# Optimization experiments

Hardware: AMD Instinct MI355X
Metric: run time of the kernel (lower is better)

## Reference

```python
import jax, jax.numpy as jnp
import numpy as np

B, T, C = 2, 4096, 768
H = 12
D = C // H  # head_size = 64


def setup_inputs() -> dict:
    key = jax.random.key(0)
    k1, k2, k3 = jax.random.split(key, 3)
    x = jax.random.normal(k1, (B, T, C), dtype=jnp.float32)
    w_attn = jax.random.normal(k2, (C, 3 * C), dtype=jnp.float32) * (C ** -0.5)
    b_attn = jnp.zeros((3 * C,), dtype=jnp.float32)
    w_proj = jax.random.normal(k3, (C, C), dtype=jnp.float32) * (C ** -0.5)
    b_proj = jnp.zeros((C,), dtype=jnp.float32)
    return {"x": x, "w_attn": w_attn, "b_attn": b_attn, "w_proj": w_proj, "b_proj": b_proj}


def reference(x, w_attn, b_attn, w_proj, b_proj):
    Bx, Tx, Cx = x.shape
    # fused QKV projection
    qkv = x @ w_attn + b_attn  # (B, T, 3C)
    q, k, v = jnp.split(qkv, 3, axis=2)
    # (B, H, T, D)
    q = q.reshape(Bx, Tx, H, D).transpose(0, 2, 1, 3)
    k = k.reshape(Bx, Tx, H, D).transpose(0, 2, 1, 3)
    v = v.reshape(Bx, Tx, H, D).transpose(0, 2, 1, 3)
    scale = 1.0 / jnp.sqrt(jnp.asarray(D, dtype=x.dtype))
    scores = jnp.einsum('bhqd,bhkd->bhqk', q, k) * scale  # (B, H, T, T)
    causal = jnp.tril(jnp.ones((Tx, Tx), dtype=bool))
    scores = jnp.where(causal, scores, jnp.asarray(-jnp.inf, dtype=scores.dtype))
    attn = jax.nn.softmax(scores, axis=-1)
    y = jnp.einsum('bhqk,bhkd->bhqd', attn, v)  # (B, H, T, D)
    y = y.transpose(0, 2, 1, 3).reshape(Bx, Tx, Cx)
    return y @ w_proj + b_proj
```

## Files before the change

kernel.cpp:

```cpp
#include <hip/hip_runtime.h>
#include <stdint.h>

#define B_   2
#define T_   4096
#define C_   768
#define H_   12
#define D_   64
#define BH_  24
#define M_   8192
#define K_   768
#define N1_  2304

#define NEG_BIG (-1.0e30f)
#define QSCALE 0.18033688011112042f

typedef short bf16x8 __attribute__((ext_vector_type(8)));
typedef float f32x4  __attribute__((ext_vector_type(4)));
typedef float f32x16 __attribute__((ext_vector_type(16)));
typedef uint32_t u32x4 __attribute__((ext_vector_type(4)));
typedef int i32x2 __attribute__((ext_vector_type(2)));

typedef const __attribute__((address_space(1))) void* as1cv;
typedef __attribute__((address_space(3))) void*       as3v;

__device__ __forceinline__ void gload_lds16(const void* g, void* l) {
  __builtin_amdgcn_global_load_lds((as1cv)g, (as3v)l, 16, 0, 0);
}

__device__ __forceinline__ unsigned short f2bf(float f) {
  uint32_t x = __builtin_bit_cast(uint32_t, f);
  uint32_t r = (x + 0x7fffu + ((x >> 16) & 1u)) >> 16;
  return (unsigned short)r;
}

__device__ __forceinline__ unsigned short f2bf_hu(float f) {
  return (unsigned short)((__builtin_bit_cast(uint32_t, f) + 0x8000u) >> 16);
}

#if __has_builtin(__builtin_amdgcn_perm)
__device__ __forceinline__ uint32_t pack_hu(float lo, float hi) {
  uint32_t a = __builtin_bit_cast(uint32_t, lo) + 0x8000u;
  uint32_t b = __builtin_bit_cast(uint32_t, hi) + 0x8000u;
  return __builtin_amdgcn_perm(b, a, 0x07060302u);
}
#else
__device__ __forceinline__ uint32_t pack_hu(float lo, float hi) {
  uint32_t a = __builtin_bit_cast(uint32_t, lo) + 0x8000u;
  uint32_t b = __builtin_bit_cast(uint32_t, hi) + 0x8000u;
  return (b & 0xFFFF0000u) | (a >> 16);
}
#endif

#if __has_builtin(__builtin_amdgcn_permlane32_swap)
#define HAVE_PLSWAP 1
#else
#define HAVE_PLSWAP 0
#endif

#if __has_builtin(__builtin_amdgcn_exp2f)
__device__ __forceinline__ float fast_exp2(float x) { return __builtin_amdgcn_exp2f(x); }
#else
__device__ __forceinline__ float fast_exp2(float x) { return __expf(x * 0.69314718056f); }
#endif

__global__ void cast_kernel(const float* __restrict__ in, unsigned short* __restrict__ out, int n4) {
  int idx = blockIdx.x * blockDim.x + threadIdx.x;
  int stride = gridDim.x * blockDim.x;
  for (int i = idx; i < n4; i += stride) {
    float4 v = reinterpret_cast<const float4*>(in)[i];
    ushort4 o;
    o.x = f2bf(v.x); o.y = f2bf(v.y); o.z = f2bf(v.z); o.w = f2bf(v.w);
    reinterpret_cast<ushort4*>(out)[i] = o;
  }
}

__global__ void transpose_cast(const float* __restrict__ in, unsigned short* __restrict__ out,
                               int K, int N) {
  __shared__ float tile[32][33];
  const int tx = threadIdx.x, ty = threadIdx.y;
  const int n = blockIdx.x * 32 + tx;
  #pragma unroll
  for (int r = 0; r < 4; ++r) {
    int k = blockIdx.y * 32 + ty + r * 8;
    tile[ty + r * 8][tx] = in[(size_t)k * N + n];
  }
  __syncthreads();
  const int k = blockIdx.y * 32 + tx;
  #pragma unroll
  for (int r = 0; r < 4; ++r) {
    int nn = blockIdx.x * 32 + ty + r * 8;
    out[(size_t)nn * K + k] = f2bf(tile[tx][ty + r * 8]);
  }
}

template <int MODE>
__global__ __launch_bounds__(256) void gemm_kernel(
    const unsigned short* __restrict__ A, const unsigned short* __restrict__ BT,
    const float* __restrict__ bias,
    unsigned short* __restrict__ o0, unsigned short* __restrict__ o1,
    unsigned short* __restrict__ o2, float* __restrict__ fo) {
  __shared__ __align__(16) unsigned short Al[128 * 32];
  __shared__ __align__(16) unsigned short Bl[128 * 32];
  const int tid = threadIdx.x;
  const int w = tid >> 6, lane = tid & 63;
  const int g = lane >> 4, c16 = lane & 15;
  const int wr = w >> 1, wc = w & 1;
  const int m0 = blockIdx.x * 128, n0 = blockIdx.y * 128;

  f32x4 acc[4][4] = {};

  for (int k0 = 0; k0 < K_; k0 += 32) {
    __syncthreads();
    #pragma unroll
    for (int q = 0; q < 2; ++q) {
      const int ch = (w * 2 + q) * 64 + lane;
      const int row = ch >> 2, kb = ch & 3;
      gload_lds16(A  + (size_t)(m0 + row) * K_ + k0 + kb * 8, &Al[(w * 2 + q) * 512]);
      gload_lds16(BT + (size_t)(n0 + row) * K_ + k0 + kb * 8, &Bl[(w * 2 + q) * 512]);
    }
    __syncthreads();
    bf16x8 af[4], bfr[4];
    #pragma unroll
    for (int i = 0; i < 4; ++i) {
      af[i]  = *reinterpret_cast<const bf16x8*>(&Al[(wr * 64 + i * 16 + c16) * 32 + g * 8]);
      bfr[i] = *reinterpret_cast<const bf16x8*>(&Bl[(wc * 64 + i * 16 + c16) * 32 + g * 8]);
    }
    #pragma unroll
    for (int i = 0; i < 4; ++i)
      #pragma unroll
      for (int j = 0; j < 4; ++j)
        acc[i][j] = __builtin_amdgcn_mfma_f32_16x16x32_bf16(af[i], bfr[j], acc[i][j], 0, 0, 0);
  }

  const int which = (MODE == 0) ? (n0 / 768) : 0;
  #pragma unroll
  for (int i = 0; i < 4; ++i) {
    const int mbase = m0 + wr * 64 + i * 16 + g * 4;
    #pragma unroll
    for (int j2 = 0; j2 < 4; ++j2) {
      const int n = n0 + wc * 64 + j2 * 16 + c16;
      const float bv = bias[n];
      #pragma unroll
      for (int j = 0; j < 4; ++j) {
        float v = acc[i][j2][j] + bv;
        const int mm = mbase + j;
        if constexpr (MODE == 0) {
          const int cc = n - which * 768;
          const int hh = cc >> 6, dd = cc & 63;
          const int bb = mm >> 12, tt = mm & 4095;
          const size_t bh = (size_t)bb * H_ + hh;
          const size_t hb = bh * T_ * D_;
          if (which == 0) {
            o0[hb + (size_t)tt * D_ + dd] = f2bf_hu(v * QSCALE);
          } else if (which == 1) {
            const int addr = ((tt >> 5) * 4 + (dd >> 4)) * 512 +
                             ((tt & 31) + ((dd >> 3) & 1) * 32) * 8 + (dd & 7);
            o1[hb + addr] = f2bf_hu(v);
          } else {
            const int addr = (tt >> 6) * 4096 + (dd >> 5) * 2048 +
                             ((tt >> 4) & 3) * 512 +
                             ((dd & 31) + ((tt >> 3) & 1) * 32) * 8 + (tt & 7);
            o2[hb + addr] = f2bf_hu(v);
          }
        } else {
          fo[(size_t)mm * 768 + n] = v;
        }
      }
    }
  }
}

__global__ __launch_bounds__(256, 2) void attn_kernel(
    const unsigned short* __restrict__ Qb, const unsigned short* __restrict__ Kb,
    const unsigned short* __restrict__ Vt, unsigned short* __restrict__ Yb) {
  __shared__ float Ml[3][64];
  __shared__ float Ll[3][64];
  __shared__ __align__(16) float Yl[3][32][64];

  const int tidx = threadIdx.x;
  const int wv = tidx >> 6;
  const int lane = tidx & 63;
  const int q31 = lane & 31, hi = lane >> 5;
  const int bid = blockIdx.x;
  const int bh = bid % BH_;
  const int strip = (T_ / 32 - 1) - bid / BH_;
  const int q0 = strip * 32;
  const int qg = q0 + q31;

  const int bb = bh / H_, hh = bh % H_;
  const size_t hoff = (size_t)bh * T_ * D_;
  const unsigned short* Qh = Qb + hoff;
  const unsigned short* Kh = Kb + hoff + lane * 8;
  const unsigned short* Vh = Vt + hoff + lane * 8;

  bf16x8 qf[4];
  #pragma unroll
  for (int s = 0; s < 4; ++s)
    qf[s] = *reinterpret_cast<const bf16x8*>(&Qh[(size_t)qg * D_ + s * 16 + hi * 8]);

  float mrun = NEG_BIG, lrun = 0.f;
  f32x16 y0 = {}, y1 = {};

  const int nt = ((q0 + 31) >> 6) + 1;

  bf16x8 kfA[8], kfB[8];

  auto tile_step = [&](bf16x8 (&kfc)[8], bf16x8 (&kfn)[8], int it) {
    const int kv0 = it << 6;

    const unsigned short* vB = Vh + it * 4096;
    bf16x8 vfA[4], vfB[4];
    #pragma unroll
    for (int ks = 0; ks < 4; ++ks) {
      vfA[ks] = *reinterpret_cast<const bf16x8*>(vB + ks * 512);
      vfB[ks] = *reinterpret_cast<const bf16x8*>(vB + 2048 + ks * 512);
    }

    const unsigned short* kN = Kh + it * 4096 + 16384;
    #pragma unroll
    for (int s = 0; s < 8; ++s)
      kfn[s] = *reinterpret_cast<const bf16x8*>(kN + (s >> 2) * 2048 + (s & 3) * 512);

    f32x16 s0 = {}, s1 = {};
    #pragma unroll
    for (int s = 0; s < 4; ++s)
      s0 = __builtin_amdgcn_mfma_f32_32x32x16_bf16(kfc[s], qf[s], s0, 0, 0, 0);
    #pragma unroll
    for (int s = 0; s < 4; ++s)
      s1 = __builtin_amdgcn_mfma_f32_32x32x16_bf16(kfc[4 + s], qf[s], s1, 0, 0, 0);

    if (kv0 + 63 > q0) {
      #pragma unroll
      for (int r = 0; r < 16; ++r) {
        const int kvl = (r & 3) + 8 * (r >> 2) + 4 * hi;
        s0[r] = (kv0 + kvl > qg)      ? NEG_BIG : s0[r];
        s1[r] = (kv0 + 32 + kvl > qg) ? NEG_BIG : s1[r];
      }
    }

    float a[16];
    #pragma unroll
    for (int r = 0; r < 8; ++r) a[r] = fmaxf(s0[2 * r], s0[2 * r + 1]);
    #pragma unroll
    for (int r = 0; r < 8; ++r) a[8 + r] = fmaxf(s1[2 * r], s1[2 * r + 1]);
    #pragma unroll
    for (int st = 8; st > 0; st >>= 1)
      #pragma unroll
      for (int r = 0; r < 16; ++r) if (r < st) a[r] = fmaxf(a[r], a[r + st]);
    float tmax = a[0];
    tmax = fmaxf(tmax, __shfl_xor(tmax, 32));

    if (__any(tmax > mrun + 11.5f)) {
      const float mnew = fmaxf(mrun, tmax);
      const float alpha = fast_exp2(mrun - mnew);
      mrun = mnew;
      lrun *= alpha;
      #pragma unroll
      for (int r = 0; r < 16; ++r) { y0[r] *= alpha; y1[r] *= alpha; }
    }

    #pragma unroll
    for (int r = 0; r < 16; ++r) {
      s0[r] = fast_exp2(s0[r] - mrun);
      s1[r] = fast_exp2(s1[r] - mrun);
    }

    #pragma unroll
    for (int r = 0; r < 8; ++r) a[r] = s0[2 * r] + s0[2 * r + 1];
    #pragma unroll
    for (int r = 0; r < 8; ++r) a[8 + r] = s1[2 * r] + s1[2 * r + 1];
    #pragma unroll
    for (int st = 8; st > 0; st >>= 1)
      #pragma unroll
      for (int r = 0; r < 16; ++r) if (r < st) a[r] = a[r] + a[r + st];
    float rsum = a[0];
    rsum += __shfl_xor(rsum, 32);
    lrun += rsum;

    bf16x8 pf[4];
#if HAVE_PLSWAP
#define MK_PF(KS, SH, GA, HA)                                                 \
    {                                                                         \
      uint32_t g0 = pack_hu(SH[(GA)*4 + 0], SH[(GA)*4 + 1]);                  \
      uint32_t g1 = pack_hu(SH[(GA)*4 + 2], SH[(GA)*4 + 3]);                  \
      uint32_t h0 = pack_hu(SH[(HA)*4 + 0], SH[(HA)*4 + 1]);                  \
      uint32_t h1 = pack_hu(SH[(HA)*4 + 2], SH[(HA)*4 + 3]);                  \
      i32x2 r0 = __builtin_amdgcn_permlane32_swap((int)g0, (int)h0, false, false); \
      i32x2 r1 = __builtin_amdgcn_permlane32_swap((int)g1, (int)h1, false, false); \
      u32x4 t;                                                                \
      t[0] = (uint32_t)r0[0];                                                 \
      t[1] = (uint32_t)r1[0];                                                 \
      t[2] = (uint32_t)r0[1];                                                 \
      t[3] = (uint32_t)r1[1];                                                 \
      pf[KS] = __builtin_bit_cast(bf16x8, t);                                 \
    }
#else
#define MK_PF(KS, SH, GA, HA)                                                 \
    {                                                                         \
      uint32_t g0 = pack_hu(SH[(GA)*4 + 0], SH[(GA)*4 + 1]);                  \
      uint32_t g1 = pack_hu(SH[(GA)*4 + 2], SH[(GA)*4 + 3]);                  \
      uint32_t h0 = pack_hu(SH[(HA)*4 + 0], SH[(HA)*4 + 1]);                  \
      uint32_t h1 = pack_hu(SH[(HA)*4 + 2], SH[(HA)*4 + 3]);                  \
      uint32_t sg0 = (uint32_t)__shfl_xor((int)g0, 32);                       \
      uint32_t sg1 = (uint32_t)__shfl_xor((int)g1, 32);                       \
      uint32_t sh0 = (uint32_t)__shfl_xor((int)h0, 32);                       \
      uint32_t sh1 = (uint32_t)__shfl_xor((int)h1, 32);                       \
      u32x4 t;                                                                \
      t[0] = hi ? sh0 : g0;                                                   \
      t[1] = hi ? sh1 : g1;                                                   \
      t[2] = hi ? h0 : sg0;                                                   \
      t[3] = hi ? h1 : sg1;                                                   \
      pf[KS] = __builtin_bit_cast(bf16x8, t);                                 \
    }
#endif
    MK_PF(0, s0, 0, 1)
    MK_PF(1, s0, 2, 3)
    MK_PF(2, s1, 0, 1)
    MK_PF(3, s1, 2, 3)
#undef MK_PF

    #pragma unroll
    for (int ks = 0; ks < 4; ++ks)
      y0 = __builtin_amdgcn_mfma_f32_32x32x16_bf16(vfA[ks], pf[ks], y0, 0, 0, 0);
    #pragma unroll
    for (int ks = 0; ks < 4; ++ks)
      y1 = __builtin_amdgcn_mfma_f32_32x32x16_bf16(vfB[ks], pf[ks], y1, 0, 0, 0);
  };

  int it = wv;
  if (it < nt) {
    #pragma unroll
    for (int s = 0; s < 8; ++s)
      kfA[s] = *reinterpret_cast<const bf16x8*>(
          Kh + (wv << 12) + (s >> 2) * 2048 + (s & 3) * 512);
    for (;;) {
      tile_step(kfA, kfB, it);
      it += 4; if (it >= nt) break;
      tile_step(kfB, kfA, it);
      it += 4; if (it >= nt) break;
    }
  }

  if (wv > 0) {
    Ml[wv - 1][lane] = mrun;
    Ll[wv - 1][lane] = lrun;
    #pragma unroll
    for (int r = 0; r < 16; ++r) {
      Yl[wv - 1][r][lane] = y0[r];
      Yl[wv - 1][16 + r][lane] = y1[r];
    }
  }
  __syncthreads();
  if (wv == 0) {
    float mp[3];
    float mm = mrun;
    #pragma unroll
    for (int p = 0; p < 3; ++p) { mp[p] = Ml[p][lane]; mm = fmaxf(mm, mp[p]); }
    const float aw = fast_exp2(mrun - mm);
    float ap[3];
    float ll = lrun * aw;
    #pragma unroll
    for (int p = 0; p < 3; ++p) {
      ap[p] = fast_exp2(mp[p] - mm);
      ll += Ll[p][lane] * ap[p];
    }
    const float inv = 1.f / ll;

    const size_t ro = ((size_t)bb * T_ + qg) * C_ + hh * D_;
    #pragma unroll
    for (int q2 = 0; q2 < 4; ++q2) {
      float v[8];
      #pragma unroll
      for (int e = 0; e < 4; ++e) {
        float t0 = y0[q2 * 4 + e] * aw;
        float t1 = y1[q2 * 4 + e] * aw;
        #pragma unroll
        for (int p = 0; p < 3; ++p) {
          t0 += Yl[p][q2 * 4 + e][lane] * ap[p];
          t1 += Yl[p][16 + q2 * 4 + e][lane] * ap[p];
        }
        v[e] = t0 * inv;
        v[4 + e] = t1 * inv;
      }
      uint2 pr0 = {pack_hu(v[0], v[1]), pack_hu(v[2], v[3])};
      *reinterpret_cast<uint2*>(&Yb[ro + q2 * 8 + hi * 4]) = pr0;
      uint2 pr1 = {pack_hu(v[4], v[5]), pack_hu(v[6], v[7])};
      *reinterpret_cast<uint2*>(&Yb[ro + 32 + q2 * 8 + hi * 4]) = pr1;
    }
  }
}

extern "C" void kernel_launch(void* const* d_in, const int* in_sizes, int n_in,
                              void* d_out, int out_size, void* d_ws, size_t ws_size,
                              hipStream_t stream) {
  const float* x      = (const float*)d_in[0];
  const float* w_attn = (const float*)d_in[1];
  const float* b_attn = (const float*)d_in[2];
  const float* w_proj = (const float*)d_in[3];
  const float* b_proj = (const float*)d_in[4];
  float* out = (float*)d_out;

  char* ws = (char*)d_ws;
  size_t off = 0;
  auto alloc = [&](size_t bytes) -> void* {
    void* p = ws + off;
    off += (bytes + 255) & ~(size_t)255;
    return p;
  };
  unsigned short* xb  = (unsigned short*)alloc((size_t)M_ * K_ * 2);
  unsigned short* waT = (unsigned short*)alloc((size_t)N1_ * K_ * 2);
  unsigned short* wpT = (unsigned short*)alloc((size_t)C_ * K_ * 2);
  unsigned short* Qb  = (unsigned short*)alloc((size_t)BH_ * T_ * D_ * 2);
  unsigned short* Kb  = (unsigned short*)alloc((size_t)BH_ * T_ * D_ * 2);
  unsigned short* Vt  = (unsigned short*)alloc((size_t)BH_ * D_ * T_ * 2);
  unsigned short* Yb  = (unsigned short*)alloc((size_t)M_ * C_ * 2);

  cast_kernel<<<1024, 256, 0, stream>>>(x, xb, M_ * K_ / 4);
  transpose_cast<<<dim3(N1_ / 32, K_ / 32), dim3(32, 8), 0, stream>>>(w_attn, waT, K_, N1_);
  transpose_cast<<<dim3(C_ / 32, K_ / 32), dim3(32, 8), 0, stream>>>(w_proj, wpT, K_, C_);

  gemm_kernel<0><<<dim3(M_ / 128, N1_ / 128), 256, 0, stream>>>(
      xb, waT, b_attn, Qb, Kb, Vt, nullptr);

  attn_kernel<<<(T_ / 32) * BH_, 256, 0, stream>>>(Qb, Kb, Vt, Yb);

  gemm_kernel<1><<<dim3(M_ / 128, C_ / 128), 256, 0, stream>>>(
      Yb, wpT, b_proj, nullptr, nullptr, nullptr, out);
}
```

Before: 186.0 us.

## Process 64 queries per attention block to reuse K/V tiles across two query groups

Each attention block now handles two 32-row query groups (64 queries) per wave, sharing every loaded K and V tile between them, and the grid is halved. This halves global K/V traffic per query and gives more MFMA work per load. It also drops the software prefetch of the next K tile, which may expose load latency, and the extra accumulators raise register pressure under the 2-blocks-per-CU launch bound. The diagonal-tile masking is specialised for the 64-row strip.

Measured after the change: 174.8 us. 1.06x faster.

```diff
diff --git a/kernel.cpp b/kernel.cpp
--- a/kernel.cpp
+++ b/kernel.cpp
@@ -173,9 +173,9 @@
 __global__ __launch_bounds__(256, 2) void attn_kernel(
     const unsigned short* __restrict__ Qb, const unsigned short* __restrict__ Kb,
     const unsigned short* __restrict__ Vt, unsigned short* __restrict__ Yb) {
-  __shared__ float Ml[3][64];
-  __shared__ float Ll[3][64];
-  __shared__ __align__(16) float Yl[3][32][64];
+  __shared__ float Ml[3][2][64];
+  __shared__ float Ll[3][2][64];
+  __shared__ __align__(16) float Yl[3][64][64];
 
   const int tidx = threadIdx.x;
   const int wv = tidx >> 6;
@@ -183,9 +183,10 @@
   const int q31 = lane & 31, hi = lane >> 5;
   const int bid = blockIdx.x;
   const int bh = bid % BH_;
-  const int strip = (T_ / 32 - 1) - bid / BH_;
-  const int q0 = strip * 32;
-  const int qg = q0 + q31;
+  const int strip = (T_ / 64 - 1) - bid / BH_;
+  const int q0 = strip * 64;
+  const int qgA = q0 + q31;
+  const int qgB = q0 + 32 + q31;
 
   const int bb = bh / H_, hh = bh % H_;
   const size_t hoff = (size_t)bh * T_ * D_;
@@ -193,199 +194,280 @@
   const unsigned short* Kh = Kb + hoff + lane * 8;
   const unsigned short* Vh = Vt + hoff + lane * 8;
 
-  bf16x8 qf[4];
+  bf16x8 qfA[4], qfB[4];
   #pragma unroll
-  for (int s = 0; s < 4; ++s)
-    qf[s] = *reinterpret_cast<const bf16x8*>(&Qh[(size_t)qg * D_ + s * 16 + hi * 8]);
-
-  float mrun = NEG_BIG, lrun = 0.f;
-  f32x16 y0 = {}, y1 = {};
-
-  const int nt = ((q0 + 31) >> 6) + 1;
-
-  bf16x8 kfA[8], kfB[8];
-
-  auto tile_step = [&](bf16x8 (&kfc)[8], bf16x8 (&kfn)[8], int it) {
+  for (int s = 0; s < 4; ++s) {
+    qfA[s] = *reinterpret_cast<const bf16x8*>(&Qh[(size_t)qgA * D_ + s * 16 + hi * 8]);
+    qfB[s] = *reinterpret_cast<const bf16x8*>(&Qh[(size_t)qgB * D_ + s * 16 + hi * 8]);
+  }
+
+  float mA = NEG_BIG, lA = 0.f, mB = NEG_BIG, lB = 0.f;
+  f32x16 yA0 = {}, yA1 = {}, yB0 = {}, yB1 = {};
+
+  const int nt = strip + 1;
+
+  for (int it = wv; it < nt; it += 4) {
     const int kv0 = it << 6;
 
-    const unsigned short* vB = Vh + it * 4096;
-    bf16x8 vfA[4], vfB[4];
+    const unsigned short* kT = Kh + it * 4096;
+    bf16x8 kf[8];
+    #pragma unroll
+    for (int s = 0; s < 8; ++s)
+      kf[s] = *reinterpret_cast<const bf16x8*>(kT + (s >> 2) * 2048 + (s & 3) * 512);
+
+    const unsigned short* vT = Vh + it * 4096;
+    bf16x8 vlo[4], vhi[4];
     #pragma unroll
     for (int ks = 0; ks < 4; ++ks) {
-      vfA[ks] = *reinterpret_cast<const bf16x8*>(vB + ks * 512);
-      vfB[ks] = *reinterpret_cast<const bf16x8*>(vB + 2048 + ks * 512);
-    }
-
-    const unsigned short* kN = Kh + it * 4096 + 16384;
-    #pragma unroll
-    for (int s = 0; s < 8; ++s)
-      kfn[s] = *reinterpret_cast<const bf16x8*>(kN + (s >> 2) * 2048 + (s & 3) * 512);
-
-    f32x16 s0 = {}, s1 = {};
-    #pragma unroll
-    for (int s = 0; s < 4; ++s)
-      s0 = __builtin_amdgcn_mfma_f32_32x32x16_bf16(kfc[s], qf[s], s0, 0, 0, 0);
-    #pragma unroll
-    for (int s = 0; s < 4; ++s)
-      s1 = __builtin_amdgcn_mfma_f32_32x32x16_bf16(kfc[4 + s], qf[s], s1, 0, 0, 0);
-
-    if (kv0 + 63 > q0) {
+      vlo[ks] = *reinterpret_cast<const bf16x8*>(vT + ks * 512);
+      vhi[ks] = *reinterpret_cast<const bf16x8*>(vT + 2048 + ks * 512);
+    }
+
+    f32x16 sA0 = {}, sA1 = {}, sB0 = {}, sB1 = {};
+    #pragma unroll
+    for (int s = 0; s < 4; ++s) {
+      sA0 = __builtin_amdgcn_mfma_f32_32x32x16_bf16(kf[s], qfA[s], sA0, 0, 0, 0);
+      sB0 = __builtin_amdgcn_mfma_f32_32x32x16_bf16(kf[s], qfB[s], sB0, 0, 0, 0);
+    }
+    #pragma unroll
+    for (int s = 0; s < 4; ++s) {
+      sA1 = __builtin_amdgcn_mfma_f32_32x32x16_bf16(kf[4 + s], qfA[s], sA1, 0, 0, 0);
+      sB1 = __builtin_amdgcn_mfma_f32_32x32x16_bf16(kf[4 + s], qfB[s], sB1, 0, 0, 0);
+    }
+
+    if (it == strip) {
       #pragma unroll
       for (int r = 0; r < 16; ++r) {
         const int kvl = (r & 3) + 8 * (r >> 2) + 4 * hi;
-        s0[r] = (kv0 + kvl > qg)      ? NEG_BIG : s0[r];
-        s1[r] = (kv0 + 32 + kvl > qg) ? NEG_BIG : s1[r];
-      }
-    }
-
-    float a[16];
-    #pragma unroll
-    for (int r = 0; r < 8; ++r) a[r] = fmaxf(s0[2 * r], s0[2 * r + 1]);
-    #pragma unroll
-    for (int r = 0; r < 8; ++r) a[8 + r] = fmaxf(s1[2 * r], s1[2 * r + 1]);
-    #pragma unroll
-    for (int st = 8; st > 0; st >>= 1)
-      #pragma unroll
-      for (int r = 0; r < 16; ++r) if (r < st) a[r] = fmaxf(a[r], a[r + st]);
-    float tmax = a[0];
-    tmax = fmaxf(tmax, __shfl_xor(tmax, 32));
-
-    if (__any(tmax > mrun + 11.5f)) {
-      const float mnew = fmaxf(mrun, tmax);
-      const float alpha = fast_exp2(mrun - mnew);
-      mrun = mnew;
-      lrun *= alpha;
-      #pragma unroll
-      for (int r = 0; r < 16; ++r) { y0[r] *= alpha; y1[r] *= alpha; }
-    }
-
-    #pragma unroll
-    for (int r = 0; r < 16; ++r) {
-      s0[r] = fast_exp2(s0[r] - mrun);
-      s1[r] = fast_exp2(s1[r] - mrun);
-    }
-
-    #pragma unroll
-    for (int r = 0; r < 8; ++r) a[r] = s0[2 * r] + s0[2 * r + 1];
-    #pragma unroll
-    for (int r = 0; r < 8; ++r) a[8 + r] = s1[2 * r] + s1[2 * r + 1];
-    #pragma unroll
-    for (int st = 8; st > 0; st >>= 1)
-      #pragma unroll
-      for (int r = 0; r < 16; ++r) if (r < st) a[r] = a[r] + a[r + st];
-    float rsum = a[0];
-    rsum += __shfl_xor(rsum, 32);
-    lrun += rsum;
-
-    bf16x8 pf[4];
+        sA0[r] = (kv0 + kvl > qgA)      ? NEG_BIG : sA0[r];
+        sA1[r] = NEG_BIG;
+        sB1[r] = (kv0 + 32 + kvl > qgB) ? NEG_BIG : sB1[r];
+      }
+    }
+
+    {
+      float a[16];
+      #pragma unroll
+      for (int r = 0; r < 8; ++r) a[r] = fmaxf(sA0[2 * r], sA0[2 * r + 1]);
+      #pragma unroll
+      for (int r = 0; r < 8; ++r) a[8 + r] = fmaxf(sA1[2 * r], sA1[2 * r + 1]);
+      #pragma unroll
+      for (int st = 8; st > 0; st >>= 1)
+        #pragma unroll
+        for (int r = 0; r < 16; ++r) if (r < st) a[r] = fmaxf(a[r], a[r + st]);
+      float tmax = a[0];
+      tmax = fmaxf(tmax, __shfl_xor(tmax, 32));
+
+      if (__any(tmax > mA + 11.5f)) {
+        const float mnew = fmaxf(mA, tmax);
+        const float alpha = fast_exp2(mA - mnew);
+        mA = mnew;
+        lA *= alpha;
+        #pragma unroll
+        for (int r = 0; r < 16; ++r) { yA0[r] *= alpha; yA1[r] *= alpha; }
+      }
+      #pragma unroll
+      for (int r = 0; r < 16; ++r) {
+        sA0[r] = fast_exp2(sA0[r] - mA);
+        sA1[r] = fast_exp2(sA1[r] - mA);
+      }
+      #pragma unroll
+      for (int r = 0; r < 8; ++r) a[r] = sA0[2 * r] + sA0[2 * r + 1];
+      #pragma unroll
+      for (int r = 0; r < 8; ++r) a[8 + r] = sA1[2 * r] + sA1[2 * r + 1];
+      #pragma unroll
+      for (int st = 8; st > 0; st >>= 1)
+        #pragma unroll
+        for (int r = 0; r < 16; ++r) if (r < st) a[r] = a[r] + a[r + st];
+      float rsum = a[0];
+      rsum += __shfl_xor(rsum, 32);
+      lA += rsum;
+
+      bf16x8 pf[4];
 #if HAVE_PLSWAP
 #define MK_PF(KS, SH, GA, HA)                                                 \
-    {                                                                         \
-      uint32_t g0 = pack_hu(SH[(GA)*4 + 0], SH[(GA)*4 + 1]);                  \
-      uint32_t g1 = pack_hu(SH[(GA)*4 + 2], SH[(GA)*4 + 3]);                  \
-      uint32_t h0 = pack_hu(SH[(HA)*4 + 0], SH[(HA)*4 + 1]);                  \
-      uint32_t h1 = pack_hu(SH[(HA)*4 + 2], SH[(HA)*4 + 3]);                  \
-      i32x2 r0 = __builtin_amdgcn_permlane32_swap((int)g0, (int)h0, false, false); \
-      i32x2 r1 = __builtin_amdgcn_permlane32_swap((int)g1, (int)h1, false, false); \
-      u32x4 t;                                                                \
-      t[0] = (uint32_t)r0[0];                                                 \
-      t[1] = (uint32_t)r1[0];                                                 \
-      t[2] = (uint32_t)r0[1];                                                 \
-      t[3] = (uint32_t)r1[1];                                                 \
-      pf[KS] = __builtin_bit_cast(bf16x8, t);                                 \
-    }
+      {                                                                       \
+        uint32_t g0 = pack_hu(SH[(GA)*4 + 0], SH[(GA)*4 + 1]);                \
+        uint32_t g1 = pack_hu(SH[(GA)*4 + 2], SH[(GA)*4 + 3]);                \
+        uint32_t h0 = pack_hu(SH[(HA)*4 + 0], SH[(HA)*4 + 1]);                \
+        uint32_t h1 = pack_hu(SH[(HA)*4 + 2], SH[(HA)*4 + 3]);                \
+        i32x2 r0 = __builtin_amdgcn_permlane32_swap((int)g0, (int)h0, false, false); \
+        i32x2 r1 = __builtin_amdgcn_permlane32_swap((int)g1, (int)h1, false, false); \
+        u32x4 t;                                                              \
+        t[0] = (uint32_t)r0[0];                                               \
+        t[1] = (uint32_t)r1[0];                                               \
+        t[2] = (uint32_t)r0[1];                                               \
+        t[3] = (uint32_t)r1[1];                                               \
+        pf[KS] = __builtin_bit_cast(bf16x8, t);                               \
+      }
 #else
 #define MK_PF(KS, SH, GA, HA)                                                 \
-    {                                                                         \
-      uint32_t g0 = pack_hu(SH[(GA)*4 + 0], SH[(GA)*4 + 1]);                  \
-      uint32_t g1 = pack_hu(SH[(GA)*4 + 2], SH[(GA)*4 + 3]);                  \
-      uint32_t h0 = pack_hu(SH[(HA)*4 + 0], SH[(HA)*4 + 1]);                  \
-      uint32_t h1 = pack_hu(SH[(HA)*4 + 2], SH[(HA)*4 + 3]);                  \
-      uint32_t sg0 = (uint32_t)__shfl_xor((int)g0, 32);                       \
-      uint32_t sg1 = (uint32_t)__shfl_xor((int)g1, 32);                       \
-      uint32_t sh0 = (uint32_t)__shfl_xor((int)h0, 32);                       \
-      uint32_t sh1 = (uint32_t)__shfl_xor((int)h1, 32);                       \
-      u32x4 t;                                                                \
-      t[0] = hi ? sh0 : g0;                                                   \
-      t[1] = hi ? sh1 : g1;                                                   \
-      t[2] = hi ? h0 : sg0;                                                   \
-      t[3] = hi ? h1 : sg1;                                                   \
-      pf[KS] = __builtin_bit_cast(bf16x8, t);                                 \
-    }
+      {                                                                       \
+        uint32_t g0 = pack_hu(SH[(GA)*4 + 0], SH[(GA)*4 + 1]);                \
+        uint32_t g1 = pack_hu(SH[(GA)*4 + 2], SH[(GA)*4 + 3]);                \
+        uint32_t h0 = pack_hu(SH[(HA)*4 + 0], SH[(HA)*4 + 1]);                \
+        uint32_t h1 = pack_hu(SH[(HA)*4 + 2], SH[(HA)*4 + 3]);                \
+        uint32_t sg0 = (uint32_t)__shfl_xor((int)g0, 32);                     \
+        uint32_t sg1 = (uint32_t)__shfl_xor((int)g1, 32);                     \
+        uint32_t sh0 = (uint32_t)__shfl_xor((int)h0, 32);                     \
+        uint32_t sh1 = (uint32_t)__shfl_xor((int)h1, 32);                     \
+        u32x4 t;                                                              \
+        t[0] = hi ? sh0 : g0;                                                 \
+        t[1] = hi ? sh1 : g1;                                                 \
+        t[2] = hi ? h0 : sg0;                                                 \
+        t[3] = hi ? h1 : sg1;                                                 \
+        pf[KS] = __builtin_bit_cast(bf16x8, t);                               \
+      }
 #endif
-    MK_PF(0, s0, 0, 1)
-    MK_PF(1, s0, 2, 3)
-    MK_PF(2, s1, 0, 1)
-    MK_PF(3, s1, 2, 3)
+      MK_PF(0, sA0, 0, 1)
+      MK_PF(1, sA0, 2, 3)
+      MK_PF(2, sA1, 0, 1)
+      MK_PF(3, sA1, 2, 3)
+
+      #pragma unroll
+      for (int ks = 0; ks < 4; ++ks)
+        yA0 = __builtin_amdgcn_mfma_f32_32x32x16_bf16(vlo[ks], pf[ks], yA0, 0, 0, 0);
+      #pragma unroll
+      for (int ks = 0; ks < 4; ++ks)
+        yA1 = __builtin_amdgcn_mfma_f32_32x32x16_bf16(vhi[ks], pf[ks], yA1, 0, 0, 0);
+    }
+
+    {
+      float a[16];
+      #pragma unroll
+      for (int r = 0; r < 8; ++r) a[r] = fmaxf(sB0[2 * r], sB0[2 * r + 1]);
+      #pragma unroll
+      for (int r = 0; r < 8; ++r) a[8 + r] = fmaxf(sB1[2 * r], sB1[2 * r + 1]);
+      #pragma unroll
+      for (int st = 8; st > 0; st >>= 1)
+        #pragma unroll
+        for (int r = 0; r < 16; ++r) if (r < st) a[r] = fmaxf(a[r], a[r + st]);
+      float tmax = a[0];
+      tmax = fmaxf(tmax, __shfl_xor(tmax, 32));
+
+      if (__any(tmax > mB + 11.5f)) {
+        const float mnew = fmaxf(mB, tmax);
+        const float alpha = fast_exp2(mB - mnew);
+        mB = mnew;
+        lB *= alpha;
+        #pragma unroll
+        for (int r = 0; r < 16; ++r) { yB0[r] *= alpha; yB1[r] *= alpha; }
+      }
+      #pragma unroll
+      for (int r = 0; r < 16; ++r) {
+        sB0[r] = fast_exp2(sB0[r] - mB);
+        sB1[r] = fast_exp2(sB1[r] - mB);
+      }
+      #pragma unroll
+      for (int r = 0; r < 8; ++r) a[r] = sB0[2 * r] + sB0[2 * r + 1];
+      #pragma unroll
+      for (int r = 0; r < 8; ++r) a[8 + r] = sB1[2 * r] + sB1[2 * r + 1];
+      #pragma unroll
+      for (int st = 8; st > 0; st >>= 1)
+        #pragma unroll
+        for (int r = 0; r < 16; ++r) if (r < st) a[r] = a[r] + a[r + st];
+      float rsum = a[0];
+      rsum += __shfl_xor(rsum, 32);
+      lB += rsum;
+
+      bf16x8 pf[4];
+      MK_PF(0, sB0, 0, 1)
+      MK_PF(1, sB0, 2, 3)
+      MK_PF(2, sB1, 0, 1)
+      MK_PF(3, sB1, 2, 3)
 #undef MK_PF
 
-    #pragma unroll
-    for (int ks = 0; ks < 4; ++ks)
-      y0 = __builtin_amdgcn_mfma_f32_32x32x16_bf16(vfA[ks], pf[ks], y0, 0, 0, 0);
-    #pragma unroll
-    for (int ks = 0; ks < 4; ++ks)
-      y1 = __builtin_amdgcn_mfma_f32_32x32x16_bf16(vfB[ks], pf[ks], y1, 0, 0, 0);
-  };
-
-  int it = wv;
-  if (it < nt) {
-    #pragma unroll
-    for (int s = 0; s < 8; ++s)
-      kfA[s] = *reinterpret_cast<const bf16x8*>(
-          Kh + (wv << 12) + (s >> 2) * 2048 + (s & 3) * 512);
-    for (;;) {
-      tile_step(kfA, kfB, it);
-      it += 4; if (it >= nt) break;
-      tile_step(kfB, kfA, it);
-      it += 4; if (it >= nt) break;
+      #pragma unroll
+      for (int ks = 0; ks < 4; ++ks)
+        yB0 = __builtin_amdgcn_mfma_f32_32x32x16_bf16(vlo[ks], pf[ks], yB0, 0, 0, 0);
+      #pragma unroll
+      for (int ks = 0; ks < 4; ++ks)
+        yB1 = __builtin_amdgcn_mfma_f32_32x32x16_bf16(vhi[ks], pf[ks], yB1, 0, 0, 0);
     }
   }
 
   if (wv > 0) {
-    Ml[wv - 1][lane] = mrun;
-    Ll[wv - 1][lane] = lrun;
+    Ml[wv - 1][0][lane] = mA; Ml[wv - 1][1][lane] = mB;
+    Ll[wv - 1][0][lane] = lA; Ll[wv - 1][1][lane] = lB;
     #pragma unroll
     for (int r = 0; r < 16; ++r) {
-      Yl[wv - 1][r][lane] = y0[r];
-      Yl[wv - 1][16 + r][lane] = y1[r];
+      Yl[wv - 1][r][lane]      = yA0[r];
+      Yl[wv - 1][16 + r][lane] = yA1[r];
+      Yl[wv - 1][32 + r][lane] = yB0[r];
+      Yl[wv - 1][48 + r][lane] = yB1[r];
     }
   }
   __syncthreads();
   if (wv == 0) {
-    float mp[3];
-    float mm = mrun;
-    #pragma unroll
-    for (int p = 0; p < 3; ++p) { mp[p] = Ml[p][lane]; mm = fmaxf(mm, mp[p]); }
-    const float aw = fast_exp2(mrun - mm);
-    float ap[3];
-    float ll = lrun * aw;
-    #pragma unroll
-    for (int p = 0; p < 3; ++p) {
-      ap[p] = fast_exp2(mp[p] - mm);
-      ll += Ll[p][lane] * ap[p];
-    }
-    const float inv = 1.f / ll;
-
-    const size_t ro = ((size_t)bb * T_ + qg) * C_ + hh * D_;
-    #pragma unroll
-    for (int q2 = 0; q2 < 4; ++q2) {
-      float v[8];
-      #pragma unroll
-      for (int e = 0; e < 4; ++e) {
-        float t0 = y0[q2 * 4 + e] * aw;
-        float t1 = y1[q2 * 4 + e] * aw;
-        #pragma unroll
-        for (int p = 0; p < 3; ++p) {
-          t0 += Yl[p][q2 * 4 + e][lane] * ap[p];
-          t1 += Yl[p][16 + q2 * 4 + e][lane] * ap[p];
+    {
+      float mm = mA;
+      #pragma unroll
+      for (int p = 0; p < 3; ++p) mm = fmaxf(mm, Ml[p][0][lane]);
+      const float aw = fast_exp2(mA - mm);
+      float ap[3];
+      float ll = lA * aw;
+      #pragma unroll
+      for (int p = 0; p < 3; ++p) {
+        ap[p] = fast_exp2(Ml[p][0][lane] - mm);
+        ll += Ll[p][0][lane] * ap[p];
+      }
+      const float inv = 1.f / ll;
+      const size_t ro = ((size_t)bb * T_ + qgA) * C_ + hh * D_;
+      #pragma unroll
+      for (int q2 = 0; q2 < 4; ++q2) {
+        float v[8];
+        #pragma unroll
+        for (int e = 0; e < 4; ++e) {
+          float t0 = yA0[q2 * 4 + e] * aw;
+          float t1 = yA1[q2 * 4 + e] * aw;
+          #pragma unroll
+          for (int p = 0; p < 3; ++p) {
+            t0 += Yl[p][q2 * 4 + e][lane] * ap[p];
+            t1 += Yl[p][16 + q2 * 4 + e][lane] * ap[p];
+          }
+          v[e] = t0 * inv;
+          v[4 + e] = t1 * inv;
         }
-        v[e] = t0 * inv;
-        v[4 + e] = t1 * inv;
-      }
-      uint2 pr0 = {pack_hu(v[0], v[1]), pack_hu(v[2], v[3])};
-      *reinterpret_cast<uint2*>(&Yb[ro + q2 * 8 + hi * 4]) = pr0;
-      uint2 pr1 = {pack_hu(v[4], v[5]), pack_hu(v[6], v[7])};
-      *reinterpret_cast<uint2*>(&Yb[ro + 32 + q2 * 8 + hi * 4]) = pr1;
+        uint2 pr0 = {pack_hu(v[0], v[1]), pack_hu(v[2], v[3])};
+        *reinterpret_cast<uint2*>(&Yb[ro + q2 * 8 + hi * 4]) = pr0;
+        uint2 pr1 = {pack_hu(v[4], v[5]), pack_hu(v[6], v[7])};
+        *reinterpret_cast<uint2*>(&Yb[ro + 32 + q2 * 8 + hi * 4]) = pr1;
+      }
+    }
+    {
+      float mm = mB;
+      #pragma unroll
+      for (int p = 0; p < 3; ++p) mm = fmaxf(mm, Ml[p][1][lane]);
+      const float aw = fast_exp2(mB - mm);
+      float ap[3];
+      float ll = lB * aw;
+      #pragma unroll
+      for (int p = 0; p < 3; ++p) {
+        ap[p] = fast_exp2(Ml[p][1][lane] - mm);
+        ll += Ll[p][1][lane] * ap[p];
+      }
+      const float inv = 1.f / ll;
+      const size_t ro = ((size_t)bb * T_ + qgB) * C_ + hh * D_;
+      #pragma unroll
+      for (int q2 = 0; q2 < 4; ++q2) {
+        float v[8];
+        #pragma unroll
+        for (int e = 0; e < 4; ++e) {
+          float t0 = yB0[q2 * 4 + e] * aw;
+          float t1 = yB1[q2 * 4 + e] * aw;
+          #pragma unroll
+          for (int p = 0; p < 3; ++p) {
+            t0 += Yl[p][32 + q2 * 4 + e][lane] * ap[p];
+            t1 += Yl[p][48 + q2 * 4 + e][lane] * ap[p];
+          }
+          v[e] = t0 * inv;
+          v[4 + e] = t1 * inv;
+        }
+        uint2 pr0 = {pack_hu(v[0], v[1]), pack_hu(v[2], v[3])};
+        *reinterpret_cast<uint2*>(&Yb[ro + q2 * 8 + hi * 4]) = pr0;
+        uint2 pr1 = {pack_hu(v[4], v[5]), pack_hu(v[6], v[7])};
+        *reinterpret_cast<uint2*>(&Yb[ro + 32 + q2 * 8 + hi * 4]) = pr1;
+      }
     }
   }
 }
@@ -422,7 +504,7 @@
   gemm_kernel<0><<<dim3(M_ / 128, N1_ / 128), 256, 0, stream>>>(
       xb, waT, b_attn, Qb, Kb, Vt, nullptr);
 
-  attn_kernel<<<(T_ / 32) * BH_, 256, 0, stream>>>(Qb, Kb, Vt, Yb);
+  attn_kernel<<<(T_ / 64) * BH_, 256, 0, stream>>>(Qb, Kb, Vt, Yb);
 
   gemm_kernel<1><<<dim3(M_ / 128, C_ / 128), 256, 0, stream>>>(
       Yb, wpT, b_proj, nullptr, nullptr, nullptr, out);
```
